# Performance work log

Hardware: AMD Instinct MI355X
Metric: run time of the kernel (lower is better)

The kernel has to match this reference:

```python
import jax, jax.numpy as jnp
import numpy as np

B, S, E, H, DK, DV, V, FH = 2, 1024, 1024, 16, 64, 64, 32000, 512


def _posenc(seq_len, d_model, n=10000.0):
    pos = jnp.arange(seq_len, dtype=jnp.float32)[:, None]            # [S,1]
    i2 = jnp.arange(0, d_model, 2, dtype=jnp.float32)                 # [E/2]
    ang = pos / jnp.power(n, i2 / d_model)                            # [S,E/2]
    return jnp.stack([jnp.sin(ang), jnp.cos(ang)], axis=-1).reshape(seq_len, d_model)


def _norm(x, g, b, eps=1e-15):
    m = jnp.mean(x, axis=-1, keepdims=True)
    v = jnp.var(x, axis=-1, keepdims=True)  # unbiased=False
    return g * (x - m) * jax.lax.rsqrt(v + eps) + b


def _ff(x, w1, b1, w2, b2):
    return jax.nn.relu(x @ w1 + b1) @ w2 + b2


def _mha(xq, xkv, wqkv, bqkv, wo, bo, causal):
    # wqkv: [3,H,E,d], bqkv: [3,H,d]  (stacked per-head linears)
    q = jnp.einsum('bse,hek->bhsk', xq, wqkv[0]) + bqkv[0][None, :, None, :]
    k = jnp.einsum('bse,hek->bhsk', xkv, wqkv[1]) + bqkv[1][None, :, None, :]
    v = jnp.einsum('bse,hev->bhsv', xkv, wqkv[2]) + bqkv[2][None, :, None, :]
    s = jnp.einsum('bhqk,bhsk->bhqs', q, k) / jnp.sqrt(jnp.float32(DK))
    if causal:
        mask = jnp.triu(jnp.ones((S, S), dtype=bool), 1)
        s = jnp.where(mask[None, None], -jnp.inf, s)
    p = jax.nn.softmax(s, axis=-1)
    o = jnp.einsum('bhqs,bhsv->bhqv', p, v)
    o = o.transpose(0, 2, 1, 3).reshape(xq.shape[0], S, H * DV)
    return o @ wo + bo


def setup_inputs():
    key = jax.random.key(0)
    ks = iter(jax.random.split(key, 40))

    def rn(shape, scale=0.02):
        return jax.random.normal(next(ks), shape, dtype=jnp.float32) * scale

    inp = {
        'src': jax.random.randint(next(ks), (B, S), 0, V, dtype=jnp.int32),
        'trg': jax.random.randint(next(ks), (B, S), 0, V, dtype=jnp.int32),
        'emb_enc': rn((V, E), 1.0),
        'emb_dec': rn((V, E), 1.0),
        'qkv_e': rn((3, H, E, DK)), 'bqkv_e': rn((3, H, DK)),
        'wo_e': rn((H * DV, E)), 'bo_e': rn((E,)),
        'qkv_m': rn((3, H, E, DK)), 'bqkv_m': rn((3, H, DK)),
        'wo_m': rn((H * DV, E)), 'bo_m': rn((E,)),
        'qkv_c': rn((3, H, E, DK)), 'bqkv_c': rn((3, H, DK)),
        'wo_c': rn((H * DV, E)), 'bo_c': rn((E,)),
        'gamma': jnp.ones((5, E), jnp.float32),
        'beta': jnp.zeros((5, E), jnp.float32),
        'ff_w1': rn((2, E, FH)), 'ff_b1': rn((2, FH)),
        'ff_w2': rn((2, FH, E)), 'ff_b2': rn((2, E)),
        'w_out': rn((E, V)), 'b_out': rn((V,)),
    }
    return inp


def reference(src, trg, emb_enc, emb_dec, qkv_e, bqkv_e, wo_e, bo_e,
              qkv_m, bqkv_m, wo_m, bo_m, qkv_c, bqkv_c, wo_c, bo_c,
              gamma, beta, ff_w1, ff_b1, ff_w2, ff_b2, w_out, b_out):
    pe = _posenc(S, E)
    # ---- encoder ----
    x = emb_enc[src] + pe
    a = _mha(x, x, qkv_e, bqkv_e, wo_e, bo_e, causal=False)
    n1 = _norm(x + a, gamma[0], beta[0])
    f = _ff(n1, ff_w1[0], ff_b1[0], ff_w2[0], ff_b2[0])
    enc = _norm(n1 + f, gamma[1], beta[1])
    # ---- decoder ----
    y = emb_dec[trg] + pe
    a = _mha(y, y, qkv_m, bqkv_m, wo_m, bo_m, causal=True)
    n1d = _norm(y + a, gamma[2], beta[2])
    a2 = _mha(n1d, enc, qkv_c, bqkv_c, wo_c, bo_c, causal=False)
    n2d = _norm(n1d + a2, gamma[3], beta[3])
    f = _ff(n2d, ff_w1[1], ff_b1[1], ff_w2[1], ff_b2[1])
    n3d = _norm(n2d + f, gamma[4], beta[4])
    logits = n3d @ w_out + b_out
    return jax.nn.softmax(logits, axis=-1)
```

## Files before the change

kernel.cpp:

```cpp
#include <hip/hip_runtime.h>
#include <hip/hip_bf16.h>
#include <hip/hip_fp16.h>
#include <math.h>

namespace {

constexpr int kB = 2, kS = 1024, kE = 1024, kH = 16, kD = 64, kV = 32000, kFH = 512;
constexpr int kBS = kB * kS;
constexpr int kHD = kH * kD;

typedef __attribute__((ext_vector_type(8))) short bf16x8;
typedef __attribute__((ext_vector_type(8))) unsigned short u16x8;
typedef __attribute__((ext_vector_type(4))) float f32x4;

#define GLDS(g, l) __builtin_amdgcn_global_load_lds(                          \
      (const __attribute__((address_space(1))) void*)(g),                     \
      (__attribute__((address_space(3))) void*)(l), 16, 0, 0)

__global__ __launch_bounds__(256) void pe_table_k(float* __restrict__ pe) {
  int s = blockIdx.x;
  float* dst = pe + (size_t)s * kE;
  for (int e = threadIdx.x; e < kE; e += 256) {
    int i = e >> 1;
    float denom = powf(10000.0f, (float)(2 * i) * (1.0f / (float)kE));
    float ang = (float)s / denom;
    dst[e] = (e & 1) ? cosf(ang) : sinf(ang);
  }
}

__global__ __launch_bounds__(256) void embed_pe_k(const int* __restrict__ tok,
                                                  const float* __restrict__ emb,
                                                  const float* __restrict__ pe,
                                                  float* __restrict__ out,
                                                  __hip_bfloat16* __restrict__ outb) {
  int row = blockIdx.x;
  int s = row & (kS - 1);
  int t = tok[row];
  const float4* src = (const float4*)(emb + (size_t)t * kE);
  const float4* per = (const float4*)(pe + (size_t)s * kE);
  float4* dst = (float4*)(out + (size_t)row * kE);
  __hip_bfloat16* dstb = outb + (size_t)row * kE;
  for (int e4 = threadIdx.x; e4 < kE / 4; e4 += 256) {
    float4 a = src[e4], p = per[e4];
    float4 v = make_float4(a.x + p.x, a.y + p.y, a.z + p.z, a.w + p.w);
    dst[e4] = v;
    union { __hip_bfloat16 h[4]; short4 s4; } u;
    u.h[0] = __float2bfloat16(v.x); u.h[1] = __float2bfloat16(v.y);
    u.h[2] = __float2bfloat16(v.z); u.h[3] = __float2bfloat16(v.w);
    ((short4*)dstb)[e4] = u.s4;
  }
}

__global__ __launch_bounds__(256) void tcast_k(const float* __restrict__ src,
                                               __hip_bfloat16* __restrict__ dst,
                                               int R, int C) {
  __shared__ float tile[32][33];
  src += (size_t)blockIdx.z * R * C;
  dst += (size_t)blockIdx.z * R * C;
  int c0 = blockIdx.x * 32, r0 = blockIdx.y * 32;
  int tx = threadIdx.x & 31, ty = threadIdx.x >> 5;
#pragma unroll
  for (int i = 0; i < 32; i += 8)
    tile[ty + i][tx] = src[(size_t)(r0 + ty + i) * C + c0 + tx];
  __syncthreads();
#pragma unroll
  for (int i = 0; i < 32; i += 8)
    dst[(size_t)(c0 + ty + i) * R + r0 + tx] = __float2bfloat16(tile[tx][ty + i]);
}

__global__ __launch_bounds__(256) void vtrans_k(const __hip_bfloat16* __restrict__ v,
                                                int sV, __hip_bfloat16* __restrict__ vt) {
  __shared__ unsigned short tile[32][34];
  int s0 = blockIdx.x * 32, d0 = blockIdx.y * 32, bh = blockIdx.z;
  int b = bh >> 4, h = bh & 15;
  int tx = threadIdx.x & 31, ty = threadIdx.x >> 5;
  const unsigned short* src = (const unsigned short*)v;
  unsigned short* dst = (unsigned short*)vt;
#pragma unroll
  for (int i = 0; i < 32; i += 8)
    tile[ty + i][tx] = src[(size_t)(b * kS + s0 + ty + i) * sV + h * 64 + d0 + tx];
  __syncthreads();
#pragma unroll
  for (int i = 0; i < 32; i += 8)
    dst[(size_t)(bh * 64 + d0 + ty + i) * kS + s0 + tx] = tile[tx][ty + i];
}

__global__ __launch_bounds__(256) void gemm_bf16_k(
    const __hip_bfloat16* __restrict__ A,
    const __hip_bfloat16* __restrict__ Bt,
    const float* __restrict__ bias,
    void* __restrict__ Cout,
    int N, int K, int mode, int gridM) {
  __shared__ __align__(16) char L[3][16384];
  const int nwg = gridDim.x, id = blockIdx.x;
  const int swz = (id & 7) * (nwg >> 3) + (id >> 3);
  const int bm = (swz % gridM) * 128, bn = (swz / gridM) * 128;
  const int tid = threadIdx.x, w = tid >> 6, lane = tid & 63;
  const int wr = w >> 1, wc = w & 1;
  const int lr = lane & 15, kg = lane >> 4;
  const int NT = K >> 5;
  const __hip_bfloat16* Ag = A + (size_t)bm * K;
  const __hip_bfloat16* Bg = Bt + (size_t)bn * K;

  auto stage = [&](int t) {
    const int buf = t % 3, k0 = t * 32;
#pragma unroll
    for (int j = 0; j < 2; ++j) {
      int slot = w * 64 + lane + j * 256;
      int row = slot >> 2;
      int cs = (slot & 3) ^ ((row >> 1) & 3);
      GLDS(Ag + (size_t)row * K + k0 + cs * 8, L[buf] + w * 1024 + j * 4096);
      GLDS(Bg + (size_t)row * K + k0 + cs * 8, L[buf] + 8192 + w * 1024 + j * 4096);
    }
  };

  f32x4 acc[4][4] = {};
  stage(0);
  stage(1);
  asm volatile("s_waitcnt vmcnt(4)" ::: "memory");
  __builtin_amdgcn_s_barrier();

  for (int t = 0; t < NT; ++t) {
    const char* buf = L[t % 3];
    if (t + 2 < NT) stage(t + 2);
    bf16x8 af[4], bfr[4];
#pragma unroll
    for (int i = 0; i < 4; ++i) {
      int row = wr * 64 + i * 16 + lr;
      af[i] = *(const bf16x8*)(buf + row * 64 + ((kg ^ ((row >> 1) & 3)) << 4));
    }
#pragma unroll
    for (int j = 0; j < 4; ++j) {
      int row = wc * 64 + j * 16 + lr;
      bfr[j] = *(const bf16x8*)(buf + 8192 + row * 64 + ((kg ^ ((row >> 1) & 3)) << 4));
    }
    __builtin_amdgcn_s_setprio(1);
#pragma unroll
    for (int i = 0; i < 4; ++i)
#pragma unroll
      for (int j = 0; j < 4; ++j)
        acc[i][j] = __builtin_amdgcn_mfma_f32_16x16x32_bf16(af[i], bfr[j], acc[i][j], 0, 0, 0);
    __builtin_amdgcn_s_setprio(0);
    if (t + 2 < NT)
      asm volatile("s_waitcnt vmcnt(4) lgkmcnt(0)" ::: "memory");
    else
      asm volatile("s_waitcnt vmcnt(0) lgkmcnt(0)" ::: "memory");
    __builtin_amdgcn_s_barrier();
  }

  float* Cf = (float*)Cout;
  __hip_bfloat16* Cb = (__hip_bfloat16*)Cout;
#pragma unroll
  for (int j = 0; j < 4; ++j) {
    int col = bn + wc * 64 + j * 16 + lr;
    float bc = bias[col];
#pragma unroll
    for (int i = 0; i < 4; ++i) {
      int rbase = bm + wr * 64 + i * 16 + kg * 4;
#pragma unroll
      for (int r = 0; r < 4; ++r) {
        float val = acc[i][j][r] + bc;
        if (mode & 1) val = fmaxf(val, 0.0f);
        if (mode < 2) Cf[(size_t)(rbase + r) * N + col] = val;
        else          Cb[(size_t)(rbase + r) * N + col] = __float2bfloat16(val);
      }
    }
  }
}

__global__ __launch_bounds__(512, 2) void gemm256_k(
    const __hip_bfloat16* __restrict__ A,
    const __hip_bfloat16* __restrict__ Bt,
    const float* __restrict__ bias,
    __half* __restrict__ C,
    int N, int K, int gridM) {
  __shared__ __align__(16) char L[3][32768];
  const int tid = threadIdx.x, w = tid >> 6, lane = tid & 63;
  const int wm = w >> 2, wn = w & 3;
  const int lr = lane & 15, kg = lane >> 4;
  const int nwg = gridDim.x, id = blockIdx.x;
  const int swz = (id & 7) * (nwg >> 3) + (id >> 3);
  const int bm = (swz % gridM) * 256, bn = (swz / gridM) * 256;
  const int NT = K >> 5;
  const __hip_bfloat16* Ag = A + (size_t)bm * K;
  const __hip_bfloat16* Bg = Bt + (size_t)bn * K;

  auto stage = [&](int t) {
    const int buf = t % 3, k0 = t * 32;
#pragma unroll
    for (int j = 0; j < 2; ++j) {
      int slot = w * 64 + lane + j * 512;
      int row = slot >> 2;
      int cs = (slot & 3) ^ ((row >> 1) & 3);
      GLDS(Ag + (size_t)row * K + k0 + cs * 8, L[buf] + w * 1024 + j * 8192);
      GLDS(Bg + (size_t)row * K + k0 + cs * 8, L[buf] + 16384 + w * 1024 + j * 8192);
    }
  };

  f32x4 acc[8][4] = {};
  stage(0);
  stage(1);
  asm volatile("s_waitcnt vmcnt(4)" ::: "memory");
  __builtin_amdgcn_s_barrier();

  for (int t = 0; t < NT; ++t) {
    const char* buf = L[t % 3];
    if (t + 2 < NT) stage(t + 2);
    bf16x8 af[8], bfr[4];
#pragma unroll
    for (int mg = 0; mg < 8; ++mg) {
      int row = wm * 128 + mg * 16 + lr;
      af[mg] = *(const bf16x8*)(buf + row * 64 + ((kg ^ ((row >> 1) & 3)) << 4));
    }
#pragma unroll
    for (int n = 0; n < 4; ++n) {
      int row = wn * 64 + n * 16 + lr;
      bfr[n] = *(const bf16x8*)(buf + 16384 + row * 64 + ((kg ^ ((row >> 1) & 3)) << 4));
    }
    __builtin_amdgcn_s_setprio(1);
#pragma unroll
    for (int mg = 0; mg < 8; ++mg)
#pragma unroll
      for (int n = 0; n < 4; ++n)
        acc[mg][n] = __builtin_amdgcn_mfma_f32_16x16x32_bf16(af[mg], bfr[n], acc[mg][n], 0, 0, 0);
    __builtin_amdgcn_s_setprio(0);
    if (t + 2 < NT)
      asm volatile("s_waitcnt vmcnt(4) lgkmcnt(0)" ::: "memory");
    else
      asm volatile("s_waitcnt vmcnt(0) lgkmcnt(0)" ::: "memory");
    __builtin_amdgcn_s_barrier();
  }

#pragma unroll
  for (int mg = 0; mg < 8; ++mg) {
    int rbase = bm + wm * 128 + mg * 16 + (kg << 2);
#pragma unroll
    for (int n = 0; n < 4; ++n) {
      int col = bn + (wn << 6) + n * 16 + lr;
      float bc = bias[col];
#pragma unroll
      for (int r = 0; r < 4; ++r)
        C[(size_t)(rbase + r) * N + col] = __float2half(acc[mg][n][r] + bc);
    }
  }
}

__global__ __launch_bounds__(256) void attn_mfma_k(
    const __hip_bfloat16* __restrict__ q, int sQ,
    const __hip_bfloat16* __restrict__ k, int sK,
    const __hip_bfloat16* __restrict__ vt,
    __hip_bfloat16* __restrict__ o,
    int causal) {
  __shared__ __align__(16) char Ks[3][8192];
  __shared__ __align__(16) char Vs[3][8192];
  __shared__ __align__(16) char Ps[4][2304];
  const int tid = threadIdx.x, w = tid >> 6, l = tid & 63;
  const int lr = l & 15, lg = l >> 4;
  const int q0 = blockIdx.x * 64, h = blockIdx.y, b = blockIdx.z;

  const int qrow = q0 + w * 16 + lr;
  const __hip_bfloat16* qp = q + (size_t)(b * kS + qrow) * sQ + h * 64 + lg * 8;
  bf16x8 aQ0 = *(const bf16x8*)qp;
  bf16x8 aQ1 = *(const bf16x8*)(qp + 32);

  f32x4 oacc[4] = {};
  float mrun[4], lrun[4];
#pragma unroll
  for (int r = 0; r < 4; ++r) { mrun[r] = -INFINITY; lrun[r] = 0.0f; }

  const int ntiles = causal ? ((q0 >> 6) + 1) : (kS >> 6);
  const int diagT = causal ? (q0 >> 6) : -1;
  const char* kbase = (const char*)(k + (size_t)(b * kS) * sK + h * 64);
  const char* vbase = (const char*)(vt + (size_t)((b * kH + h) * 64) * kS);
  char* Pw = Ps[w];

  auto stage = [&](int t) {
    const int buf = t % 3, kv0 = t * 64;
#pragma unroll
    for (int i = 0; i < 2; ++i) {
      int slot = w * 128 + i * 64 + l;
      int row = slot >> 3, sl = slot & 7, c = sl ^ (row & 7);
      GLDS(kbase + (size_t)(kv0 + row) * sK * 2 + c * 16, Ks[buf] + (w * 128 + i * 64) * 16);
      GLDS(vbase + (size_t)row * kS * 2 + kv0 * 2 + c * 16, Vs[buf] + (w * 128 + i * 64) * 16);
    }
  };

  stage(0);
  if (ntiles > 1) {
    stage(1);
    asm volatile("s_waitcnt vmcnt(4)" ::: "memory");
  } else {
    asm volatile("s_waitcnt vmcnt(0)" ::: "memory");
  }
  __builtin_amdgcn_s_barrier();

  for (int t = 0; t < ntiles; ++t) {
    const int kv0 = t * 64;
    const char* Kb = Ks[t % 3];
    const char* Vb = Vs[t % 3];
    if (t + 2 < ntiles) stage(t + 2);

    f32x4 sacc[4] = {};
#pragma unroll
    for (int nf = 0; nf < 4; ++nf) {
      int key = nf * 16 + lr;
#pragma unroll
      for (int kf = 0; kf < 2; ++kf) {
        int ch = (lg + kf * 4) ^ (key & 7);
        bf16x8 bK = *(const bf16x8*)(Kb + key * 128 + ch * 16);
        sacc[nf] = __builtin_amdgcn_mfma_f32_16x16x32_bf16(kf ? aQ1 : aQ0, bK, sacc[nf], 0, 0, 0);
      }
    }

#pragma unroll
    for (int r = 0; r < 4; ++r) {
      int row16 = lg * 4 + r;
      int qg = q0 + w * 16 + row16;
      float sv[4];
#pragma unroll
      for (int nf = 0; nf < 4; ++nf) {
        float s = sacc[nf][r] * 0.125f;
        if (t == diagT && (kv0 + nf * 16 + lr) > qg) s = -INFINITY;
        sv[nf] = s;
      }
      float mx = fmaxf(fmaxf(sv[0], sv[1]), fmaxf(sv[2], sv[3]));
#pragma unroll
      for (int m = 1; m < 16; m <<= 1) mx = fmaxf(mx, __shfl_xor(mx, m));
      float mnew = fmaxf(mrun[r], mx);
      float sc = __expf(mrun[r] - mnew);
      mrun[r] = mnew;
      float rs = 0.0f;
#pragma unroll
      for (int nf = 0; nf < 4; ++nf) {
        float p = __expf(sv[nf] - mnew);
        rs += p;
        *(__hip_bfloat16*)(Pw + row16 * 144 + (nf * 16 + lr) * 2) = __float2bfloat16(p);
      }
#pragma unroll
      for (int m = 1; m < 16; m <<= 1) rs += __shfl_xor(rs, m);
      lrun[r] = lrun[r] * sc + rs;
#pragma unroll
      for (int nfd = 0; nfd < 4; ++nfd) oacc[nfd][r] *= sc;
    }

    bf16x8 aP0 = *(const bf16x8*)(Pw + lr * 144 + (lg * 8) * 2);
    bf16x8 aP1 = *(const bf16x8*)(Pw + lr * 144 + (lg * 8 + 32) * 2);
#pragma unroll
    for (int nfd = 0; nfd < 4; ++nfd) {
      int d = nfd * 16 + lr;
#pragma unroll
      for (int kf = 0; kf < 2; ++kf) {
        int ch = (lg + kf * 4) ^ (d & 7);
        bf16x8 bV = *(const bf16x8*)(Vb + d * 128 + ch * 16);
        oacc[nfd] = __builtin_amdgcn_mfma_f32_16x16x32_bf16(kf ? aP1 : aP0, bV, oacc[nfd], 0, 0, 0);
      }
    }

    if (t + 1 < ntiles) {
      if (t + 2 < ntiles)
        asm volatile("s_waitcnt vmcnt(4) lgkmcnt(0)" ::: "memory");
      else
        asm volatile("s_waitcnt vmcnt(0) lgkmcnt(0)" ::: "memory");
      __builtin_amdgcn_s_barrier();
    }
  }

#pragma unroll
  for (int r = 0; r < 4; ++r) {
    float inv = 1.0f / lrun[r];
    int rowg = q0 + w * 16 + lg * 4 + r;
#pragma unroll
    for (int nfd = 0; nfd < 4; ++nfd)
      o[(size_t)(b * kS + rowg) * kHD + h * 64 + nfd * 16 + lr] =
          __float2bfloat16(oacc[nfd][r] * inv);
  }
}

__global__ __launch_bounds__(256) void ln_res_k(const float* __restrict__ a,
                                                const float* __restrict__ b,
                                                const float* __restrict__ gamma,
                                                const float* __restrict__ beta,
                                                float* __restrict__ out,
                                                __hip_bfloat16* __restrict__ outb) {
  __shared__ float sh[10];
  int row = blockIdx.x, tid = threadIdx.x;
  const float4* a4 = (const float4*)(a + (size_t)row * kE);
  const float4* b4 = (const float4*)(b + (size_t)row * kE);
  float4 t = a4[tid], u = b4[tid];
  t.x += u.x; t.y += u.y; t.z += u.z; t.w += u.w;
  float s = t.x + t.y + t.z + t.w;
  float q2 = t.x * t.x + t.y * t.y + t.z * t.z + t.w * t.w;
  for (int o = 32; o > 0; o >>= 1) { s += __shfl_down(s, o); q2 += __shfl_down(q2, o); }
  int lane = tid & 63, wid = tid >> 6;
  if (lane == 0) { sh[wid] = s; sh[4 + wid] = q2; }
  __syncthreads();
  if (tid == 0) {
    float S2 = sh[0] + sh[1] + sh[2] + sh[3];
    float Q2 = sh[4] + sh[5] + sh[6] + sh[7];
    float mean = S2 * (1.0f / kE);
    float var = Q2 * (1.0f / kE) - mean * mean;
    sh[8] = mean;
    sh[9] = rsqrtf(var + 1e-15f);
  }
  __syncthreads();
  float mean = sh[8], inv = sh[9];
  float4 g = ((const float4*)gamma)[tid], be = ((const float4*)beta)[tid];
  float4 v;
  v.x = g.x * ((t.x - mean) * inv) + be.x;
  v.y = g.y * ((t.y - mean) * inv) + be.y;
  v.z = g.z * ((t.z - mean) * inv) + be.z;
  v.w = g.w * ((t.w - mean) * inv) + be.w;
  ((float4*)(out + (size_t)row * kE))[tid] = v;
  union { __hip_bfloat16 h[4]; short4 s4; } uo;
  uo.h[0] = __float2bfloat16(v.x); uo.h[1] = __float2bfloat16(v.y);
  uo.h[2] = __float2bfloat16(v.z); uo.h[3] = __float2bfloat16(v.w);
  ((short4*)(outb + (size_t)row * kE))[tid] = uo.s4;
}

__global__ __launch_bounds__(512) void softmax_rows_k(const __half* __restrict__ lgt,
                                                      float* __restrict__ out) {
  __shared__ float sh[18];
  int row = blockIdx.x;
  const u16x8* x8 = (const u16x8*)(lgt + (size_t)row * kV);
  const int n8 = kV / 8;
  int tid = threadIdx.x;
  u16x8 v[8];
  float m = -INFINITY, sum = 0.0f;
#pragma unroll
  for (int i = 0; i < 8; ++i) {
    int idx = tid + i * 512;
    if (idx < n8) {
      v[i] = x8[idx];
      union { u16x8 u; __half h[8]; } cv; cv.u = v[i];
      float f[8];
#pragma unroll
      for (int j = 0; j < 8; ++j) f[j] = __half2float(cv.h[j]);
      float mx = f[0];
#pragma unroll
      for (int j = 1; j < 8; ++j) mx = fmaxf(mx, f[j]);
      float nm = fmaxf(m, mx);
      float add = 0.0f;
#pragma unroll
      for (int j = 0; j < 8; ++j) add += __expf(f[j] - nm);
      sum = sum * __expf(m - nm) + add;
      m = nm;
    }
  }
  for (int o = 32; o > 0; o >>= 1) {
    float om = __shfl_down(m, o), os = __shfl_down(sum, o);
    float nm = fmaxf(m, om);
    sum = sum * __expf(m - nm) + os * __expf(om - nm);
    m = nm;
  }
  int lane = tid & 63, wid = tid >> 6;
  if (lane == 0) { sh[wid] = m; sh[8 + wid] = sum; }
  __syncthreads();
  if (tid == 0) {
    float M = sh[0], S2 = 0.0f;
#pragma unroll
    for (int i2 = 1; i2 < 8; ++i2) M = fmaxf(M, sh[i2]);
#pragma unroll
    for (int i2 = 0; i2 < 8; ++i2) S2 += sh[8 + i2] * __expf(sh[i2] - M);
    sh[16] = M;
    sh[17] = 1.0f / S2;
  }
  __syncthreads();
  float M = sh[16], rcp = sh[17];
#pragma unroll
  for (int i = 0; i < 8; ++i) {
    int idx = tid + i * 512;
    if (idx < n8) {
      union { u16x8 u; __half h[8]; } cv; cv.u = v[i];
      float4 o0, o1;
      o0.x = __expf(__half2float(cv.h[0]) - M) * rcp;
      o0.y = __expf(__half2float(cv.h[1]) - M) * rcp;
      o0.z = __expf(__half2float(cv.h[2]) - M) * rcp;
      o0.w = __expf(__half2float(cv.h[3]) - M) * rcp;
      o1.x = __expf(__half2float(cv.h[4]) - M) * rcp;
      o1.y = __expf(__half2float(cv.h[5]) - M) * rcp;
      o1.z = __expf(__half2float(cv.h[6]) - M) * rcp;
      o1.w = __expf(__half2float(cv.h[7]) - M) * rcp;
      float* dst = out + (size_t)row * kV + idx * 8;
      ((float4*)dst)[0] = o0;
      ((float4*)dst)[1] = o1;
    }
  }
}

}

extern "C" void kernel_launch(void* const* d_in, const int* in_sizes, int n_in,
                              void* d_out, int out_size, void* d_ws, size_t ws_size,
                              hipStream_t stream) {
  const int*   src    = (const int*)d_in[0];
  const int*   trg    = (const int*)d_in[1];
  const float* emb_e  = (const float*)d_in[2];
  const float* emb_d  = (const float*)d_in[3];
  const float* qkv_e  = (const float*)d_in[4];
  const float* bqkv_e = (const float*)d_in[5];
  const float* wo_e   = (const float*)d_in[6];
  const float* bo_e   = (const float*)d_in[7];
  const float* qkv_m  = (const float*)d_in[8];
  const float* bqkv_m = (const float*)d_in[9];
  const float* wo_m   = (const float*)d_in[10];
  const float* bo_m   = (const float*)d_in[11];
  const float* qkv_c  = (const float*)d_in[12];
  const float* bqkv_c = (const float*)d_in[13];
  const float* wo_c   = (const float*)d_in[14];
  const float* bo_c   = (const float*)d_in[15];
  const float* gamma  = (const float*)d_in[16];
  const float* beta   = (const float*)d_in[17];
  const float* ffw1   = (const float*)d_in[18];
  const float* ffb1   = (const float*)d_in[19];
  const float* ffw2   = (const float*)d_in[20];
  const float* ffb2   = (const float*)d_in[21];
  const float* wout   = (const float*)d_in[22];
  const float* bout   = (const float*)d_in[23];
  float* out = (float*)d_out;

  char* base = (char*)d_ws;
  const size_t R = (size_t)kBS * kE;
  float* enc_x = (float*)base;
  float* dec_x = enc_x + R;
  float* t1    = dec_x + R;
  float* n1    = t1 + R;
  float* n_enc = n1 + R;
  __hip_bfloat16* bb     = (__hip_bfloat16*)(n_enc + R);
  __hip_bfloat16* enc_xb = bb;
  __hip_bfloat16* n1b    = enc_xb + R;
  __hip_bfloat16* n_encb = n1b + R;
  __hip_bfloat16* qkvb   = n_encb + R;
  __hip_bfloat16* kvb    = qkvb + 3 * R;
  __hip_bfloat16* qb1    = kvb + 2 * R;
  __hip_bfloat16* vtb    = qb1 + R;
  __hip_bfloat16* ao16   = vtb + R;
  __hip_bfloat16* ffhb   = ao16 + R;
  __hip_bfloat16* Wqkv   = ffhb + R / 2;
  __hip_bfloat16* Wo     = Wqkv + (size_t)3 * kHD * kE;
  __hip_bfloat16* Wf1 = Wo + (size_t)kE * kHD;
  __hip_bfloat16* Wf2 = Wf1 + (size_t)kFH * kE;
  const size_t lgtBytes = (size_t)kBS * kV * sizeof(__half);
  __hip_bfloat16* dec_xb = (__hip_bfloat16*)(base + lgtBytes);
  __hip_bfloat16* Wv     = dec_xb + R;
  __half* lgt = (__half*)base;
  float* pe = (float*)Wv;

  auto tcast = [&](const float* s, __hip_bfloat16* d, int Rr, int Cc, int batch) {
    tcast_k<<<dim3(Cc / 32, Rr / 32, batch), 256, 0, stream>>>(s, d, Rr, Cc);
  };
  auto gemmb = [&](const __hip_bfloat16* A, const __hip_bfloat16* Bt, const float* bias,
                   void* C, int M, int N, int K, int mode) {
    int gridM = M / 128;
    gemm_bf16_k<<<dim3(gridM * (N / 128)), 256, 0, stream>>>(A, Bt, bias, C, N, K, mode, gridM);
  };
  auto vtrans = [&](const __hip_bfloat16* v, int sV) {
    vtrans_k<<<dim3(kS / 32, kD / 32, kB * kH), 256, 0, stream>>>(v, sV, vtb);
  };
  auto attn = [&](const __hip_bfloat16* q, int sQ, const __hip_bfloat16* k, int sK,
                  int causal) {
    attn_mfma_k<<<dim3(kS / 64, kH, kB), 256, 0, stream>>>(q, sQ, k, sK, vtb, ao16, causal);
  };
  auto ln = [&](const float* a, const float* b2, int sel, float* o1, __hip_bfloat16* o2) {
    ln_res_k<<<kBS, 256, 0, stream>>>(a, b2, gamma + sel * kE, beta + sel * kE, o1, o2);
  };

  pe_table_k<<<kS, 256, 0, stream>>>(pe);

  embed_pe_k<<<kBS, 256, 0, stream>>>(src, emb_e, pe, enc_x, enc_xb);
  tcast(qkv_e, Wqkv, kE, kD, 3 * kH);
  tcast(wo_e, Wo, kHD, kE, 1);
  gemmb(enc_xb, Wqkv, bqkv_e, qkvb, kBS, 3 * kHD, kE, 2);
  vtrans(qkvb + 2 * kHD, 3 * kHD);
  attn(qkvb, 3 * kHD, qkvb + kHD, 3 * kHD, 0);
  gemmb(ao16, Wo, bo_e, t1, kBS, kE, kHD, 0);
  ln(enc_x, t1, 0, n1, n1b);
  tcast(ffw1, Wf1, kE, kFH, 1);
  tcast(ffw2, Wf2, kFH, kE, 1);
  gemmb(n1b, Wf1, ffb1, ffhb, kBS, kFH, kE, 3);
  gemmb(ffhb, Wf2, ffb2, t1, kBS, kE, kFH, 0);
  ln(n1, t1, 1, n_enc, n_encb);

  embed_pe_k<<<kBS, 256, 0, stream>>>(trg, emb_d, pe, dec_x, dec_xb);
  tcast(qkv_m, Wqkv, kE, kD, 3 * kH);
  tcast(wo_m, Wo, kHD, kE, 1);
  gemmb(dec_xb, Wqkv, bqkv_m, qkvb, kBS, 3 * kHD, kE, 2);
  vtrans(qkvb + 2 * kHD, 3 * kHD);
  attn(qkvb, 3 * kHD, qkvb + kHD, 3 * kHD, 1);
  gemmb(ao16, Wo, bo_m, t1, kBS, kE, kHD, 0);
  ln(dec_x, t1, 2, n1, n1b);

  tcast(qkv_c, Wqkv, kE, kD, 3 * kH);
  tcast(wo_c, Wo, kHD, kE, 1);
  gemmb(n1b, Wqkv, bqkv_c, qb1, kBS, kHD, kE, 2);
  gemmb(n_encb, Wqkv + (size_t)kHD * kE, bqkv_c + kHD, kvb, kBS, 2 * kHD, kE, 2);
  vtrans(kvb + kHD, 2 * kHD);
  attn(qb1, kHD, kvb, 2 * kHD, 0);
  gemmb(ao16, Wo, bo_c, t1, kBS, kE, kHD, 0);
  ln(n1, t1, 3, enc_x, enc_xb);

  tcast(ffw1 + (size_t)kE * kFH, Wf1, kE, kFH, 1);
  tcast(ffw2 + (size_t)kFH * kE, Wf2, kFH, kE, 1);
  gemmb(enc_xb, Wf1, ffb1 + kFH, ffhb, kBS, kFH, kE, 3);
  gemmb(ffhb, Wf2, ffb2 + kE, t1, kBS, kE, kFH, 0);
  ln(enc_x, t1, 4, dec_x, dec_xb);

  tcast(wout, Wv, kE, kV, 1);
  gemm256_k<<<dim3((kBS / 256) * (kV / 256)), 512, 0, stream>>>(
      dec_xb, Wv, bout, lgt, kV, kE, kBS / 256);
  softmax_rows_k<<<kBS, 512, 0, stream>>>(lgt, out);
}
```

Before: 666.6 us.

## Use 4 waves with 128x128 per-wave tiles in vocab GEMM

Restructures the 256x256-tile output-projection GEMM from 8 waves (128x64 each) to 4 waves (128x128 each), doubling accumulators per wave to 8x8 MFMA tiles. It also moves the LDS fragment reads ahead of issuing the next stage's global-to-LDS loads. The aim is more MFMA work per LDS read and fewer waves contending for LDS bandwidth. In exchange each wave holds 256 accumulator registers, which lowers occupancy and leaves fewer waves to hide load latency, with a risk of register spills.

```diff
diff --git a/kernel.cpp b/kernel.cpp
--- a/kernel.cpp
+++ b/kernel.cpp
@@ -168,7 +168,7 @@
   }
 }
 
-__global__ __launch_bounds__(512, 2) void gemm256_k(
+__global__ __launch_bounds__(256, 1) void gemm256_k(
     const __hip_bfloat16* __restrict__ A,
     const __hip_bfloat16* __restrict__ Bt,
     const float* __restrict__ bias,
@@ -176,7 +176,7 @@
     int N, int K, int gridM) {
   __shared__ __align__(16) char L[3][32768];
   const int tid = threadIdx.x, w = tid >> 6, lane = tid & 63;
-  const int wm = w >> 2, wn = w & 3;
+  const int wr = w >> 1, wc = w & 1;
   const int lr = lane & 15, kg = lane >> 4;
   const int nwg = gridDim.x, id = blockIdx.x;
   const int swz = (id & 7) * (nwg >> 3) + (id >> 3);
@@ -188,59 +188,59 @@
   auto stage = [&](int t) {
     const int buf = t % 3, k0 = t * 32;
 #pragma unroll
-    for (int j = 0; j < 2; ++j) {
-      int slot = w * 64 + lane + j * 512;
+    for (int j = 0; j < 4; ++j) {
+      int slot = tid + j * 256;
       int row = slot >> 2;
       int cs = (slot & 3) ^ ((row >> 1) & 3);
-      GLDS(Ag + (size_t)row * K + k0 + cs * 8, L[buf] + w * 1024 + j * 8192);
-      GLDS(Bg + (size_t)row * K + k0 + cs * 8, L[buf] + 16384 + w * 1024 + j * 8192);
-    }
-  };
-
-  f32x4 acc[8][4] = {};
+      GLDS(Ag + (size_t)row * K + k0 + cs * 8, L[buf] + slot * 16);
+      GLDS(Bg + (size_t)row * K + k0 + cs * 8, L[buf] + 16384 + slot * 16);
+    }
+  };
+
+  f32x4 acc[8][8] = {};
   stage(0);
   stage(1);
-  asm volatile("s_waitcnt vmcnt(4)" ::: "memory");
+  asm volatile("s_waitcnt vmcnt(8)" ::: "memory");
   __builtin_amdgcn_s_barrier();
 
   for (int t = 0; t < NT; ++t) {
     const char* buf = L[t % 3];
+    bf16x8 af[8], bfr[8];
+#pragma unroll
+    for (int i = 0; i < 8; ++i) {
+      int row = wr * 128 + i * 16 + lr;
+      af[i] = *(const bf16x8*)(buf + row * 64 + ((kg ^ ((row >> 1) & 3)) << 4));
+    }
+#pragma unroll
+    for (int j = 0; j < 8; ++j) {
+      int row = wc * 128 + j * 16 + lr;
+      bfr[j] = *(const bf16x8*)(buf + 16384 + row * 64 + ((kg ^ ((row >> 1) & 3)) << 4));
+    }
     if (t + 2 < NT) stage(t + 2);
-    bf16x8 af[8], bfr[4];
-#pragma unroll
-    for (int mg = 0; mg < 8; ++mg) {
-      int row = wm * 128 + mg * 16 + lr;
-      af[mg] = *(const bf16x8*)(buf + row * 64 + ((kg ^ ((row >> 1) & 3)) << 4));
-    }
-#pragma unroll
-    for (int n = 0; n < 4; ++n) {
-      int row = wn * 64 + n * 16 + lr;
-      bfr[n] = *(const bf16x8*)(buf + 16384 + row * 64 + ((kg ^ ((row >> 1) & 3)) << 4));
-    }
     __builtin_amdgcn_s_setprio(1);
 #pragma unroll
-    for (int mg = 0; mg < 8; ++mg)
-#pragma unroll
-      for (int n = 0; n < 4; ++n)
-        acc[mg][n] = __builtin_amdgcn_mfma_f32_16x16x32_bf16(af[mg], bfr[n], acc[mg][n], 0, 0, 0);
+    for (int i = 0; i < 8; ++i)
+#pragma unroll
+      for (int j = 0; j < 8; ++j)
+        acc[i][j] = __builtin_amdgcn_mfma_f32_16x16x32_bf16(af[i], bfr[j], acc[i][j], 0, 0, 0);
     __builtin_amdgcn_s_setprio(0);
     if (t + 2 < NT)
-      asm volatile("s_waitcnt vmcnt(4) lgkmcnt(0)" ::: "memory");
+      asm volatile("s_waitcnt vmcnt(8) lgkmcnt(0)" ::: "memory");
     else
       asm volatile("s_waitcnt vmcnt(0) lgkmcnt(0)" ::: "memory");
     __builtin_amdgcn_s_barrier();
   }
 
 #pragma unroll
-  for (int mg = 0; mg < 8; ++mg) {
-    int rbase = bm + wm * 128 + mg * 16 + (kg << 2);
-#pragma unroll
-    for (int n = 0; n < 4; ++n) {
-      int col = bn + (wn << 6) + n * 16 + lr;
+  for (int i = 0; i < 8; ++i) {
+    int rbase = bm + wr * 128 + i * 16 + (kg << 2);
+#pragma unroll
+    for (int j = 0; j < 8; ++j) {
+      int col = bn + wc * 128 + j * 16 + lr;
       float bc = bias[col];
 #pragma unroll
       for (int r = 0; r < 4; ++r)
-        C[(size_t)(rbase + r) * N + col] = __float2half(acc[mg][n][r] + bc);
+        C[(size_t)(rbase + r) * N + col] = __float2half(acc[i][j][r] + bc);
     }
   }
 }
@@ -605,7 +605,7 @@
   ln(enc_x, t1, 4, dec_x, dec_xb);
 
   tcast(wout, Wv, kE, kV, 1);
-  gemm256_k<<<dim3((kBS / 256) * (kV / 256)), 512, 0, stream>>>(
+  gemm256_k<<<dim3((kBS / 256) * (kV / 256)), 256, 0, stream>>>(
       dec_xb, Wv, bout, lgt, kV, kE, kBS / 256);
   softmax_rows_k<<<kBS, 512, 0, stream>>>(lgt, out);
 }
```

Measured after the change: 700.2 us. 5.0% more time.
